# Performance work log

Measured on AMD Instinct MI355X. Metric: run time of the kernel, lower is better.

## Reference

```python
import jax, jax.numpy as jnp
import numpy as np

NUM_HEADS, NUM_KV_HEADS, HEAD_DIM, HIDDEN = 8, 1, 256, 2048
B, S = 1, 4096

def setup_inputs() -> dict:
    key = jax.random.key(0)
    ks = jax.random.split(key, 6)
    sd = 1.0 / np.sqrt(HIDDEN)
    x = jax.random.normal(ks[0], (B, S, HIDDEN), dtype=jnp.float32)
    wq = jax.random.normal(ks[1], (HIDDEN, NUM_HEADS, HEAD_DIM), dtype=jnp.float32) * sd
    bq = jnp.zeros((NUM_HEADS, HEAD_DIM), dtype=jnp.float32)
    wkv = jax.random.normal(ks[2], (HIDDEN, NUM_KV_HEADS, HEAD_DIM), dtype=jnp.float32) * sd
    bkv = jnp.zeros((NUM_KV_HEADS, HEAD_DIM), dtype=jnp.float32)
    wo = jax.random.normal(ks[3], (NUM_HEADS, HEAD_DIM, HIDDEN), dtype=jnp.float32) / np.sqrt(NUM_HEADS * HEAD_DIM)
    bo = jnp.zeros((HIDDEN,), dtype=jnp.float32)
    # causal mask, broadcastable to [b, h, q, k]
    mask = jnp.tril(jnp.ones((S, S), dtype=bool))[None, None, :, :]
    return {"x": x, "wq": wq, "bq": bq, "wkv": wkv, "bkv": bkv, "wo": wo, "bo": bo, "mask": mask}

def reference(x, wq, bq, wkv, bkv, wo, bo, mask):
    # q: [b,s,h,d]; kv: [b,s,kvh,d] -- used as BOTH k and v (as in source)
    q = jnp.einsum('bsh,hnd->bsnd', x, wq) + bq
    kv = jnp.einsum('bsh,hnd->bsnd', x, wkv) + bkv
    q = jnp.transpose(q, (0, 2, 1, 3))   # [b,h,s,d]
    k = jnp.transpose(kv, (0, 2, 1, 3))  # [b,kvh,s,d]
    v = k
    rep = NUM_HEADS // NUM_KV_HEADS
    k = jnp.repeat(k, rep, axis=1)
    v = jnp.repeat(v, rep, axis=1)
    scale = 1.0 / jnp.sqrt(jnp.float32(HEAD_DIM))
    attn = jnp.einsum('bhqd,bhkd->bhqk', q, k) * scale
    attn = jnp.where(mask, attn, -1e9)
    attn = jax.nn.softmax(attn, axis=-1)
    out = jnp.einsum('bhqk,bhkd->bhqd', attn, v)
    out = jnp.transpose(out, (0, 2, 1, 3))  # [b,s,h,d]
    return jnp.einsum('bsnd,ndh->bsh', out, wo) + bo
```

## Files before the change

kernel.cpp:

```cpp
#include <hip/hip_runtime.h>
#include <hip/hip_bf16.h>
#include <stdint.h>

#define HIDDEN 2048
#define SEQ 4096
#define NH 8
#define HD 256

typedef float f32x4 __attribute__((ext_vector_type(4)));
typedef short s16x8 __attribute__((ext_vector_type(8)));
typedef float f32x4v __attribute__((ext_vector_type(4)));
typedef unsigned int u32x2 __attribute__((ext_vector_type(2)));

#define QSCALE 0.09016844005556021f

__device__ inline uint16_t f2bf(float f) {
  union { float f; uint32_t u; } v;
  v.f = f;
  uint32_t r = (v.u + 0x7fffu + ((v.u >> 16) & 1u)) >> 16;
  return (uint16_t)r;
}

__device__ inline uint32_t cvtpk(float a, float b) {
  uint32_t r;
  asm("v_cvt_pk_bf16_f32 %0, %1, %2" : "=v"(r) : "v"(a), "v"(b));
  return r;
}

__device__ inline void gll16(const uint16_t* src, uint16_t* lds) {
  __builtin_amdgcn_global_load_lds(
      (const __attribute__((address_space(1))) unsigned int*)src,
      (__attribute__((address_space(3))) unsigned int*)lds, 16, 0, 0);
}

__global__ __launch_bounds__(256) void cast_kernel(const float* __restrict__ in,
                                                   uint16_t* __restrict__ out, int n4) {
  int i = blockIdx.x * 256 + threadIdx.x;
  if (i >= n4) return;
  f32x4v v = ((const f32x4v*)in)[i];
  union { uint16_t u[4]; uint64_t l; } o;
  o.u[0] = f2bf(v.x); o.u[1] = f2bf(v.y); o.u[2] = f2bf(v.z); o.u[3] = f2bf(v.w);
  ((uint64_t*)out)[i] = o.l;
}

__global__ __launch_bounds__(256) void transpose_cast_kernel(const float* __restrict__ in,
                                                             uint16_t* __restrict__ out,
                                                             int R, int C) {
  __shared__ uint16_t tile[64][65];
  int t = threadIdx.x;
  int ctiles = C >> 6;
  int c0 = (blockIdx.x % ctiles) << 6;
  int r0 = (blockIdx.x / ctiles) << 6;
#pragma unroll
  for (int p = 0; p < 16; ++p) {
    int r = p * 4 + (t >> 6), c = t & 63;
    tile[c][r] = f2bf(in[(size_t)(r0 + r) * C + c0 + c]);
  }
  __syncthreads();
#pragma unroll
  for (int p = 0; p < 16; ++p) {
    int r = p * 4 + (t >> 6), c = t & 63;
    out[(size_t)(c0 + r) * R + r0 + c] = tile[r][c];
  }
}

__device__ inline void gemm_tile_core(const uint16_t* __restrict__ A,
                                      const uint16_t* __restrict__ BT, int K, int m0,
                                      uint16_t* Alds, uint16_t* Blds, f32x4 acc[4][4]) {
  const int t = threadIdx.x, lane = t & 63, wid = t >> 6;
  const int l15 = lane & 15, l4 = lane >> 4;
  const int wm = wid >> 1, wn = wid & 1;
#pragma unroll
  for (int i = 0; i < 4; ++i)
#pragma unroll
    for (int j = 0; j < 4; ++j) acc[i][j] = f32x4{0.f, 0.f, 0.f, 0.f};

  auto stage = [&](int kt, int b) {
#pragma unroll
    for (int i = 0; i < 2; ++i) {
      int j = i * 256 + t;
      gll16(A + (size_t)(m0 + (j >> 2)) * K + kt + (j & 3) * 8,
            Alds + b * 4096 + (i * 256 + wid * 64) * 8);
    }
#pragma unroll
    for (int i = 0; i < 2; ++i) {
      int j = i * 256 + t;
      gll16(BT + (size_t)(j >> 2) * K + kt + (j & 3) * 8,
            Blds + b * 4096 + (i * 256 + wid * 64) * 8);
    }
  };

  stage(0, 0);
  int b = 0;
  for (int kt = 0; kt < K; kt += 32, b ^= 1) {
    __syncthreads();
    if (kt + 32 < K) stage(kt + 32, b ^ 1);
    s16x8 av[4], bv[4];
#pragma unroll
    for (int mi = 0; mi < 4; ++mi)
      av[mi] = *(const s16x8*)(Alds + b * 4096 + (wm * 64 + mi * 16 + l15) * 32 + l4 * 8);
#pragma unroll
    for (int nj = 0; nj < 4; ++nj)
      bv[nj] = *(const s16x8*)(Blds + b * 4096 + (wn * 64 + nj * 16 + l15) * 32 + l4 * 8);
#pragma unroll
    for (int mi = 0; mi < 4; ++mi)
#pragma unroll
      for (int nj = 0; nj < 4; ++nj)
        acc[mi][nj] = __builtin_amdgcn_mfma_f32_16x16x32_bf16(av[mi], bv[nj],
                                                              acc[mi][nj], 0, 0, 0);
  }
}

__global__ __launch_bounds__(256) void gemm_qkv_kernel(
    const uint16_t* __restrict__ xb, const uint16_t* __restrict__ wqT,
    const uint16_t* __restrict__ wkvT, const float* __restrict__ bq,
    const float* __restrict__ bkv, uint16_t* __restrict__ Qws,
    uint16_t* __restrict__ Kws, uint16_t* __restrict__ VTws) {
  __shared__ uint16_t Alds[8192], Blds[8192];
  int b0 = blockIdx.x;
  int bid = (b0 & 7) * 72 + (b0 >> 3);
  int bn = bid % 18, bm = bid / 18;
  int m0 = bm * 128;
  const uint16_t* BT = (bn < 16) ? (wqT + (size_t)bn * 128 * HIDDEN)
                                 : (wkvT + (size_t)(bn - 16) * 128 * HIDDEN);
  f32x4 acc[4][4];
  gemm_tile_core(xb, BT, HIDDEN, m0, Alds, Blds, acc);
  const int lane = threadIdx.x & 63, wid = threadIdx.x >> 6;
  const int l15 = lane & 15, l4 = lane >> 4;
  const int wm = wid >> 1, wn = wid & 1;
#pragma unroll
  for (int mi = 0; mi < 4; ++mi) {
#pragma unroll
    for (int nj = 0; nj < 4; ++nj) {
      int nloc = bn * 128 + wn * 64 + nj * 16 + l15;
#pragma unroll
      for (int r = 0; r < 4; ++r) {
        int m = m0 + wm * 64 + mi * 16 + 4 * l4 + r;
        float v = acc[mi][nj][r];
        if (bn < 16) {
          v = (v + bq[nloc]) * QSCALE;
          uint16_t b = f2bf(v);
          int head = nloc >> 8, d = nloc & 255;
          Qws[((size_t)head * SEQ + m) * HD + d] = b;
        } else {
          int d = nloc - 2048;
          v += bkv[d];
          uint16_t b = f2bf(v);
          Kws[(size_t)m * HD + d] = b;
          VTws[(size_t)d * SEQ + m] = b;
        }
      }
    }
  }
}

__global__ __launch_bounds__(256) void attn_kernel(const uint16_t* __restrict__ Qws,
                                                   const uint16_t* __restrict__ Kws,
                                                   const uint16_t* __restrict__ VTws,
                                                   uint16_t* __restrict__ Ows) {
  __shared__ unsigned char smem[74752];
  uint16_t* Klds = (uint16_t*)smem;
  uint16_t* VTlds = (uint16_t*)(smem + 32768);
  const int t = threadIdx.x, lane = t & 63, wid = t >> 6;
  const int l15 = lane & 15, l4 = lane >> 4;
  const int b = blockIdx.x;
  const int h = b & 7, p = (b >> 3) & 31;
  const int qb = (b < 256) ? (63 - p) : p;
  const int qrow = qb * 64 + wid * 16 + l15;
  uint16_t* Pw = (uint16_t*)(smem + 65536 + wid * 2304);

  int koff[8];
#pragma unroll
  for (int kk = 0; kk < 8; ++kk) {
    int c = kk * 4 + l4;
    int cs = (c & ~7) | ((c ^ l15) & 7);
    koff[kk] = l15 * 512 + cs * 16;
  }
  int voff[2];
#pragma unroll
  for (int kk = 0; kk < 2; ++kk) {
    int c = (kk * 4 + l4) ^ (l15 & 7);
    voff[kk] = l15 * 128 + c * 16;
  }

  auto stageKV = [&](int kb) {
#pragma unroll
    for (int i = 0; i < 8; ++i) {
      int j = i * 256 + t;
      int r = j >> 5, cp = j & 31;
      int c = (cp & ~7) | ((cp ^ r) & 7);
      gll16(Kws + (size_t)(kb * 64 + r) * HD + c * 8, Klds + (i * 256 + wid * 64) * 8);
    }
#pragma unroll
    for (int i = 0; i < 8; ++i) {
      int j = i * 256 + t;
      int d = j >> 3, cp = j & 7;
      int c = (cp ^ d) & 7;
      gll16(VTws + (size_t)d * SEQ + kb * 64 + c * 8, VTlds + (i * 256 + wid * 64) * 8);
    }
  };

  s16x8 qf[8];
  const uint16_t* qbase = Qws + ((size_t)h * SEQ + qrow) * HD;
#pragma unroll
  for (int kk = 0; kk < 8; ++kk) qf[kk] = *(const s16x8*)(qbase + kk * 32 + l4 * 8);

  float mrun = -1e30f, lrun = 0.f;
  f32x4 oacc[16];
#pragma unroll
  for (int i = 0; i < 16; ++i) oacc[i] = f32x4{0.f, 0.f, 0.f, 0.f};

  const int nt = qb + 1;
  stageKV(0);

  for (int kb = 0; kb < nt; ++kb) {
    __syncthreads();

    f32x4 sacc[4];
#pragma unroll
    for (int i = 0; i < 4; ++i) sacc[i] = f32x4{0.f, 0.f, 0.f, 0.f};
#pragma unroll
    for (int kvt = 0; kvt < 4; ++kvt) {
#pragma unroll
      for (int kk = 0; kk < 8; ++kk) {
        s16x8 kf = *(const s16x8*)((const unsigned char*)Klds + kvt * 8192 + koff[kk]);
        sacc[kvt] = __builtin_amdgcn_mfma_f32_16x16x32_bf16(kf, qf[kk], sacc[kvt], 0, 0, 0);
      }
    }

    float pv[16];
    float vmax = -1e30f;
    const bool diag = (kb == qb);
#pragma unroll
    for (int kvt = 0; kvt < 4; ++kvt) {
#pragma unroll
      for (int r = 0; r < 4; ++r) {
        float s = sacc[kvt][r];
        if (diag) {
          int kv = kb * 64 + kvt * 16 + 4 * l4 + r;
          if (kv > qrow) s = -1e30f;
        }
        pv[kvt * 4 + r] = s;
        vmax = fmaxf(vmax, s);
      }
    }
    vmax = fmaxf(vmax, __shfl_xor(vmax, 16));
    vmax = fmaxf(vmax, __shfl_xor(vmax, 32));

    if (!__all(vmax - mrun <= 8.0f)) {
      float mnew = fmaxf(mrun, vmax);
      float alpha = exp2f(mrun - mnew);
      float a4[4];
#pragma unroll
      for (int r = 0; r < 4; ++r) a4[r] = __shfl(alpha, 4 * l4 + r);
#pragma unroll
      for (int dt = 0; dt < 16; ++dt) {
#pragma unroll
        for (int r = 0; r < 4; ++r) oacc[dt][r] *= a4[r];
      }
      lrun *= alpha;
      mrun = mnew;
    }
    float rsum = 0.f;
#pragma unroll
    for (int i = 0; i < 16; ++i) {
      float pe = exp2f(pv[i] - mrun);
      pv[i] = pe;
      rsum += pe;
    }
    rsum += __shfl_xor(rsum, 16);
    rsum += __shfl_xor(rsum, 32);
    lrun += rsum;

#pragma unroll
    for (int kvt = 0; kvt < 4; ++kvt) {
      u32x2 w;
      w.x = cvtpk(pv[kvt * 4 + 0], pv[kvt * 4 + 1]);
      w.y = cvtpk(pv[kvt * 4 + 2], pv[kvt * 4 + 3]);
      *(u32x2*)(Pw + l15 * 72 + kvt * 16 + l4 * 4) = w;
    }
#pragma unroll
    for (int kk = 0; kk < 2; ++kk) {
      s16x8 pa = *(const s16x8*)(Pw + l15 * 72 + kk * 32 + l4 * 8);
#pragma unroll
      for (int dt = 0; dt < 16; ++dt) {
        s16x8 vf = *(const s16x8*)((const unsigned char*)VTlds + dt * 2048 + voff[kk]);
        oacc[dt] = __builtin_amdgcn_mfma_f32_16x16x32_bf16(pa, vf, oacc[dt], 0, 0, 0);
      }
    }

    if (kb + 1 < nt) {
      __syncthreads();
      stageKV(kb + 1);
    }
  }

  float linv = 1.0f / lrun;
  float li4[4];
#pragma unroll
  for (int r = 0; r < 4; ++r) li4[r] = __shfl(linv, 4 * l4 + r);
#pragma unroll
  for (int dt = 0; dt < 16; ++dt) {
#pragma unroll
    for (int r = 0; r < 4; ++r) {
      int s = qb * 64 + wid * 16 + 4 * l4 + r;
      int col = h * HD + dt * 16 + l15;
      Ows[(size_t)s * HIDDEN + col] = f2bf(oacc[dt][r] * li4[r]);
    }
  }
}

__global__ __launch_bounds__(256) void gemm_out_kernel(const uint16_t* __restrict__ Ows,
                                                       const uint16_t* __restrict__ woT,
                                                       const float* __restrict__ bo,
                                                       float* __restrict__ Y) {
  __shared__ uint16_t Alds[8192], Blds[8192];
  int b0 = blockIdx.x;
  int bid = (b0 & 7) * 64 + (b0 >> 3);
  int bn = bid % 16, bm = bid / 16;
  int m0 = bm * 128;
  f32x4 acc[4][4];
  gemm_tile_core(Ows, woT + (size_t)bn * 128 * HIDDEN, HIDDEN, m0, Alds, Blds, acc);
  const int lane = threadIdx.x & 63, wid = threadIdx.x >> 6;
  const int l15 = lane & 15, l4 = lane >> 4;
  const int wm = wid >> 1, wn = wid & 1;
#pragma unroll
  for (int mi = 0; mi < 4; ++mi) {
#pragma unroll
    for (int nj = 0; nj < 4; ++nj) {
      int n = bn * 128 + wn * 64 + nj * 16 + l15;
      float bias = bo[n];
#pragma unroll
      for (int r = 0; r < 4; ++r) {
        int m = m0 + wm * 64 + mi * 16 + 4 * l4 + r;
        Y[(size_t)m * HIDDEN + n] = acc[mi][nj][r] + bias;
      }
    }
  }
}

extern "C" void kernel_launch(void* const* d_in, const int* in_sizes, int n_in,
                              void* d_out, int out_size, void* d_ws, size_t ws_size,
                              hipStream_t stream) {
  const float* x = (const float*)d_in[0];
  const float* wq = (const float*)d_in[1];
  const float* bq = (const float*)d_in[2];
  const float* wkv = (const float*)d_in[3];
  const float* bkv = (const float*)d_in[4];
  const float* wo = (const float*)d_in[5];
  const float* bo = (const float*)d_in[6];
  float* Y = (float*)d_out;

  uint8_t* ws = (uint8_t*)d_ws;
  uint16_t* xb   = (uint16_t*)(ws + 0);
  uint16_t* wqT  = (uint16_t*)(ws + 16777216);
  uint16_t* wkvT = (uint16_t*)(ws + 25165824);
  uint16_t* woT  = (uint16_t*)(ws + 26214400);
  uint16_t* Qws  = (uint16_t*)(ws + 34603008);
  uint16_t* Kws  = (uint16_t*)(ws + 51380224);
  uint16_t* VTws = (uint16_t*)(ws + 53477376);
  uint16_t* Ows  = (uint16_t*)(ws + 55574528);

  cast_kernel<<<8192, 256, 0, stream>>>(x, xb, (SEQ * HIDDEN) / 4);
  transpose_cast_kernel<<<1024, 256, 0, stream>>>(wq, wqT, HIDDEN, 2048);
  transpose_cast_kernel<<<128, 256, 0, stream>>>(wkv, wkvT, HIDDEN, 256);
  transpose_cast_kernel<<<1024, 256, 0, stream>>>(wo, woT, 2048, HIDDEN);
  gemm_qkv_kernel<<<32 * 18, 256, 0, stream>>>(xb, wqT, wkvT, bq, bkv, Qws, Kws, VTws);
  attn_kernel<<<512, 256, 0, stream>>>(Qws, Kws, VTws, Ows);
  gemm_out_kernel<<<32 * 16, 256, 0, stream>>>(Ows, woT, bo, Y);
}
```

Before: 486.2 us.

## Pair causal q-blocks per workgroup, double-buffer K in LDS, load V directly

The attention kernel now runs 256 workgroups, and each processes two query blocks (63-p and p) one after the other, so every workgroup gets the same total causal work. K tiles are double-buffered in LDS and the next tile is prefetched while the current one is computed. V^T fragments are read straight from global memory into registers (32 vectors per thread) instead of being staged through LDS. This aims to balance load and overlap loads with compute, but it halves the grid, adds register pressure from holding V fragments, and relies on uncoalesced global V reads going through cache.

Measured after the change: 571.4 us. +17.5%, slower.

```diff
diff --git a/kernel.cpp b/kernel.cpp
--- a/kernel.cpp
+++ b/kernel.cpp
@@ -159,14 +159,9 @@
                                                    const uint16_t* __restrict__ VTws,
                                                    uint16_t* __restrict__ Ows) {
   __shared__ unsigned char smem[74752];
-  uint16_t* Klds = (uint16_t*)smem;
-  uint16_t* VTlds = (uint16_t*)(smem + 32768);
   const int t = threadIdx.x, lane = t & 63, wid = t >> 6;
   const int l15 = lane & 15, l4 = lane >> 4;
-  const int b = blockIdx.x;
-  const int h = b & 7, p = (b >> 3) & 31;
-  const int qb = (b < 256) ? (63 - p) : p;
-  const int qrow = qb * 64 + wid * 16 + l15;
+  const int h = blockIdx.x & 7, p = blockIdx.x >> 3;
   uint16_t* Pw = (uint16_t*)(smem + 65536 + wid * 2304);
 
   int koff[8];
@@ -176,14 +171,9 @@
     int cs = (c & ~7) | ((c ^ l15) & 7);
     koff[kk] = l15 * 512 + cs * 16;
   }
-  int voff[2];
-#pragma unroll
-  for (int kk = 0; kk < 2; ++kk) {
-    int c = (kk * 4 + l4) ^ (l15 & 7);
-    voff[kk] = l15 * 128 + c * 16;
-  }
-
-  auto stageKV = [&](int kb) {
+
+  auto stageK = [&](int kb, int buf) {
+    uint16_t* Klds = (uint16_t*)(smem + buf * 32768);
 #pragma unroll
     for (int i = 0; i < 8; ++i) {
       int j = i * 256 + t;
@@ -191,121 +181,130 @@
       int c = (cp & ~7) | ((cp ^ r) & 7);
       gll16(Kws + (size_t)(kb * 64 + r) * HD + c * 8, Klds + (i * 256 + wid * 64) * 8);
     }
-#pragma unroll
-    for (int i = 0; i < 8; ++i) {
-      int j = i * 256 + t;
-      int d = j >> 3, cp = j & 7;
-      int c = (cp ^ d) & 7;
-      gll16(VTws + (size_t)d * SEQ + kb * 64 + c * 8, VTlds + (i * 256 + wid * 64) * 8);
-    }
   };
 
-  s16x8 qf[8];
-  const uint16_t* qbase = Qws + ((size_t)h * SEQ + qrow) * HD;
-#pragma unroll
-  for (int kk = 0; kk < 8; ++kk) qf[kk] = *(const s16x8*)(qbase + kk * 32 + l4 * 8);
-
-  float mrun = -1e30f, lrun = 0.f;
-  f32x4 oacc[16];
-#pragma unroll
-  for (int i = 0; i < 16; ++i) oacc[i] = f32x4{0.f, 0.f, 0.f, 0.f};
-
-  const int nt = qb + 1;
-  stageKV(0);
-
-  for (int kb = 0; kb < nt; ++kb) {
+  for (int half = 0; half < 2; ++half) {
+    const int qb = half ? p : 63 - p;
+    const int qrow = qb * 64 + wid * 16 + l15;
+
+    s16x8 qf[8];
+    const uint16_t* qbase = Qws + ((size_t)h * SEQ + qrow) * HD;
+#pragma unroll
+    for (int kk = 0; kk < 8; ++kk) qf[kk] = *(const s16x8*)(qbase + kk * 32 + l4 * 8);
+
+    float mrun = -1e30f, lrun = 0.f;
+    f32x4 oacc[16];
+#pragma unroll
+    for (int i = 0; i < 16; ++i) oacc[i] = f32x4{0.f, 0.f, 0.f, 0.f};
+
+    const int nt = qb + 1;
     __syncthreads();
-
-    f32x4 sacc[4];
-#pragma unroll
-    for (int i = 0; i < 4; ++i) sacc[i] = f32x4{0.f, 0.f, 0.f, 0.f};
-#pragma unroll
-    for (int kvt = 0; kvt < 4; ++kvt) {
-#pragma unroll
-      for (int kk = 0; kk < 8; ++kk) {
-        s16x8 kf = *(const s16x8*)((const unsigned char*)Klds + kvt * 8192 + koff[kk]);
-        sacc[kvt] = __builtin_amdgcn_mfma_f32_16x16x32_bf16(kf, qf[kk], sacc[kvt], 0, 0, 0);
-      }
-    }
-
-    float pv[16];
-    float vmax = -1e30f;
-    const bool diag = (kb == qb);
-#pragma unroll
-    for (int kvt = 0; kvt < 4; ++kvt) {
+    stageK(0, 0);
+
+    for (int kb = 0; kb < nt; ++kb) {
+      const int buf = kb & 1;
+      __syncthreads();
+      if (kb + 1 < nt) stageK(kb + 1, buf ^ 1);
+
+      s16x8 vf[32];
+#pragma unroll
+      for (int dt = 0; dt < 16; ++dt) {
+#pragma unroll
+        for (int kk = 0; kk < 2; ++kk) {
+          vf[dt * 2 + kk] = *(const s16x8*)(VTws + (size_t)(dt * 16 + l15) * SEQ +
+                                            kb * 64 + (kk * 4 + l4) * 8);
+        }
+      }
+
+      const unsigned char* Klds = (const unsigned char*)(smem + buf * 32768);
+      f32x4 sacc[4];
+#pragma unroll
+      for (int i = 0; i < 4; ++i) sacc[i] = f32x4{0.f, 0.f, 0.f, 0.f};
+#pragma unroll
+      for (int kvt = 0; kvt < 4; ++kvt) {
+#pragma unroll
+        for (int kk = 0; kk < 8; ++kk) {
+          s16x8 kf = *(const s16x8*)(Klds + kvt * 8192 + koff[kk]);
+          sacc[kvt] = __builtin_amdgcn_mfma_f32_16x16x32_bf16(kf, qf[kk], sacc[kvt], 0, 0, 0);
+        }
+      }
+
+      float pv[16];
+      float vmax = -1e30f;
+      const bool diag = (kb == qb);
+#pragma unroll
+      for (int kvt = 0; kvt < 4; ++kvt) {
+#pragma unroll
+        for (int r = 0; r < 4; ++r) {
+          float s = sacc[kvt][r];
+          if (diag) {
+            int kv = kb * 64 + kvt * 16 + 4 * l4 + r;
+            if (kv > qrow) s = -1e30f;
+          }
+          pv[kvt * 4 + r] = s;
+          vmax = fmaxf(vmax, s);
+        }
+      }
+      vmax = fmaxf(vmax, __shfl_xor(vmax, 16));
+      vmax = fmaxf(vmax, __shfl_xor(vmax, 32));
+
+      if (!__all(vmax - mrun <= 8.0f)) {
+        float mnew = fmaxf(mrun, vmax);
+        float alpha = exp2f(mrun - mnew);
+        float a4[4];
+#pragma unroll
+        for (int r = 0; r < 4; ++r) a4[r] = __shfl(alpha, 4 * l4 + r);
+#pragma unroll
+        for (int dt = 0; dt < 16; ++dt) {
+#pragma unroll
+          for (int r = 0; r < 4; ++r) oacc[dt][r] *= a4[r];
+        }
+        lrun *= alpha;
+        mrun = mnew;
+      }
+      float rsum = 0.f;
+#pragma unroll
+      for (int i = 0; i < 16; ++i) {
+        float pe = exp2f(pv[i] - mrun);
+        pv[i] = pe;
+        rsum += pe;
+      }
+      rsum += __shfl_xor(rsum, 16);
+      rsum += __shfl_xor(rsum, 32);
+      lrun += rsum;
+
+#pragma unroll
+      for (int kvt = 0; kvt < 4; ++kvt) {
+        u32x2 w;
+        w.x = cvtpk(pv[kvt * 4 + 0], pv[kvt * 4 + 1]);
+        w.y = cvtpk(pv[kvt * 4 + 2], pv[kvt * 4 + 3]);
+        *(u32x2*)(Pw + l15 * 72 + kvt * 16 + l4 * 4) = w;
+      }
+      s16x8 pa[2];
+#pragma unroll
+      for (int kk = 0; kk < 2; ++kk)
+        pa[kk] = *(const s16x8*)(Pw + l15 * 72 + kk * 32 + l4 * 8);
+#pragma unroll
+      for (int dt = 0; dt < 16; ++dt) {
+#pragma unroll
+        for (int kk = 0; kk < 2; ++kk)
+          oacc[dt] = __builtin_amdgcn_mfma_f32_16x16x32_bf16(pa[kk], vf[dt * 2 + kk],
+                                                             oacc[dt], 0, 0, 0);
+      }
+    }
+
+    float linv = 1.0f / lrun;
+    float li4[4];
+#pragma unroll
+    for (int r = 0; r < 4; ++r) li4[r] = __shfl(linv, 4 * l4 + r);
+#pragma unroll
+    for (int dt = 0; dt < 16; ++dt) {
 #pragma unroll
       for (int r = 0; r < 4; ++r) {
-        float s = sacc[kvt][r];
-        if (diag) {
-          int kv = kb * 64 + kvt * 16 + 4 * l4 + r;
-          if (kv > qrow) s = -1e30f;
-        }
-        pv[kvt * 4 + r] = s;
-        vmax = fmaxf(vmax, s);
-      }
-    }
-    vmax = fmaxf(vmax, __shfl_xor(vmax, 16));
-    vmax = fmaxf(vmax, __shfl_xor(vmax, 32));
-
-    if (!__all(vmax - mrun <= 8.0f)) {
-      float mnew = fmaxf(mrun, vmax);
-      float alpha = exp2f(mrun - mnew);
-      float a4[4];
-#pragma unroll
-      for (int r = 0; r < 4; ++r) a4[r] = __shfl(alpha, 4 * l4 + r);
-#pragma unroll
-      for (int dt = 0; dt < 16; ++dt) {
-#pragma unroll
-        for (int r = 0; r < 4; ++r) oacc[dt][r] *= a4[r];
-      }
-      lrun *= alpha;
-      mrun = mnew;
-    }
-    float rsum = 0.f;
-#pragma unroll
-    for (int i = 0; i < 16; ++i) {
-      float pe = exp2f(pv[i] - mrun);
-      pv[i] = pe;
-      rsum += pe;
-    }
-    rsum += __shfl_xor(rsum, 16);
-    rsum += __shfl_xor(rsum, 32);
-    lrun += rsum;
-
-#pragma unroll
-    for (int kvt = 0; kvt < 4; ++kvt) {
-      u32x2 w;
-      w.x = cvtpk(pv[kvt * 4 + 0], pv[kvt * 4 + 1]);
-      w.y = cvtpk(pv[kvt * 4 + 2], pv[kvt * 4 + 3]);
-      *(u32x2*)(Pw + l15 * 72 + kvt * 16 + l4 * 4) = w;
-    }
-#pragma unroll
-    for (int kk = 0; kk < 2; ++kk) {
-      s16x8 pa = *(const s16x8*)(Pw + l15 * 72 + kk * 32 + l4 * 8);
-#pragma unroll
-      for (int dt = 0; dt < 16; ++dt) {
-        s16x8 vf = *(const s16x8*)((const unsigned char*)VTlds + dt * 2048 + voff[kk]);
-        oacc[dt] = __builtin_amdgcn_mfma_f32_16x16x32_bf16(pa, vf, oacc[dt], 0, 0, 0);
-      }
-    }
-
-    if (kb + 1 < nt) {
-      __syncthreads();
-      stageKV(kb + 1);
-    }
-  }
-
-  float linv = 1.0f / lrun;
-  float li4[4];
-#pragma unroll
-  for (int r = 0; r < 4; ++r) li4[r] = __shfl(linv, 4 * l4 + r);
-#pragma unroll
-  for (int dt = 0; dt < 16; ++dt) {
-#pragma unroll
-    for (int r = 0; r < 4; ++r) {
-      int s = qb * 64 + wid * 16 + 4 * l4 + r;
-      int col = h * HD + dt * 16 + l15;
-      Ows[(size_t)s * HIDDEN + col] = f2bf(oacc[dt][r] * li4[r]);
+        int s = qb * 64 + wid * 16 + 4 * l4 + r;
+        int col = h * HD + dt * 16 + l15;
+        Ows[(size_t)s * HIDDEN + col] = f2bf(oacc[dt][r] * li4[r]);
+      }
     }
   }
 }
@@ -366,6 +365,6 @@
   transpose_cast_kernel<<<128, 256, 0, stream>>>(wkv, wkvT, HIDDEN, 256);
   transpose_cast_kernel<<<1024, 256, 0, stream>>>(wo, woT, 2048, HIDDEN);
   gemm_qkv_kernel<<<32 * 18, 256, 0, stream>>>(xb, wqT, wkvT, bq, bkv, Qws, Kws, VTws);
-  attn_kernel<<<512, 256, 0, stream>>>(Qws, Kws, VTws, Ows);
+  attn_kernel<<<256, 256, 0, stream>>>(Qws, Kws, VTws, Ows);
   gemm_out_kernel<<<32 * 16, 256, 0, stream>>>(Ows, woT, bo, Y);
 }
```
